# Optimization experiments

Hardware: AMD Instinct MI355X
Metric: run time of the kernel (lower is better)

The kernel has to match this reference:

```python
import jax, jax.numpy as jnp
import numpy as np
from math import factorial


def _su2_cg(j1, j2, j3, m1, m2, m3):
    # Complex SU(2) Clebsch-Gordan coefficient <j1 m1; j2 m2 | j3 m3> (Condon-Shortley),
    # same formula as e3nn's _su2_clebsch_gordan_coeff.
    if m3 != m1 + m2:
        return 0.0
    f = factorial
    vmin = max(-j1 + j2 + m3, -j1 + m1, 0)
    vmax = min(j2 + j3 + m1, j3 - j1 + j2, j3 + m3)
    C = ((2 * j3 + 1) * f(j3 + j1 - j2) * f(j3 - j1 + j2) * f(j1 + j2 - j3) / f(j1 + j2 + j3 + 1)
         * f(j3 + m3) * f(j3 - m3) / (f(j1 - m1) * f(j1 + m1) * f(j2 - m2) * f(j2 + m2))) ** 0.5
    S = 0.0
    for v in range(vmin, vmax + 1):
        S += (-1.0) ** (v + j2 + m2) / f(v) * f(j2 + j3 + m1 - v) * f(j1 - m1 + v) / (
            f(j3 - j1 + j2 - v) * f(j3 + m3 - v) * f(v + j1 - j2 - m3))
    return C * S


def _q(l):
    # Change of basis real -> complex spherical harmonics (e3nn convention).
    q = np.zeros((2 * l + 1, 2 * l + 1), dtype=np.complex128)
    for m in range(-l, 0):
        q[l + m, l + abs(m)] = 1 / 2 ** 0.5
        q[l + m, l - abs(m)] = -1j / 2 ** 0.5
    q[l, l] = 1
    for m in range(1, l + 1):
        q[l + m, l + abs(m)] = (-1) ** m / 2 ** 0.5
        q[l + m, l - abs(m)] = 1j * (-1) ** m / 2 ** 0.5
    return (-1j) ** l * q


def _w3j(l1, l2, l3):
    # Real Wigner-3j-like invariant tensor, Frobenius norm 1 (e3nn wigner_3j).
    C = np.zeros((2 * l1 + 1, 2 * l2 + 1, 2 * l3 + 1), dtype=np.complex128)
    for m1 in range(-l1, l1 + 1):
        for m2 in range(-l2, l2 + 1):
            m3 = m1 + m2
            if -l3 <= m3 <= l3:
                C[l1 + m1, l2 + m2, l3 + m3] = _su2_cg(l1, l2, l3, m1, m2, m3)
    C = np.einsum('ij,kl,mn,ikn->jlm', _q(l1), _q(l2), np.conj(_q(l3).T), C)
    C = np.real(C)
    return C / np.linalg.norm(C)


def _cg_full():
    # 1o x 1o -> 0e + 1e + 2e. e3nn FullTensorProduct ('uuu', component norm,
    # element path norm, mul=1) gives path_weight = sqrt(2*l_out + 1) per path.
    return np.concatenate([(2 * l + 1) ** 0.5 * _w3j(1, 1, l) for l in range(3)],
                          axis=-1).astype(np.float32)  # [3, 3, 9]


def setup_inputs() -> dict:
    key = jax.random.key(0)
    N = 8388608  # 2**23 rows, ~96 MB input
    frac = jax.random.normal(key, (N, 3), dtype=jnp.float32)
    cg = jnp.asarray(_cg_full())  # [3, 3, 9] fixed Clebsch-Gordan constants
    return {"frac": frac, "cg": cg}


def reference(frac, cg):
    # SimpleTP.forward: tp(frac, frac) -> [N, 9], then sum over dim 0 -> [9].
    # Fused segment-wise CG contraction + batch reduction in one einsum.
    return jnp.einsum('ni,nj,ijk->k', frac, frac, cg)
```

## Files before the change

kernel.cpp:

```cpp
#include <hip/hip_runtime.h>


constexpr int BLK  = 256;
constexpr int GRID = 2048;
constexpr int WPB  = BLK / 64;
constexpr long NWAVES = (long)GRID * WPB;

#define ACC6(x, y, z)                                              \
    do {                                                           \
        s00 = fmaf((x), (x), s00); s01 = fmaf((x), (y), s01);      \
        s02 = fmaf((x), (z), s02); s11 = fmaf((y), (y), s11);      \
        s12 = fmaf((y), (z), s12); s22 = fmaf((z), (z), s22);      \
    } while (0)

__global__ __launch_bounds__(BLK) void tp_partial(const float* __restrict__ frac,
                                                  float* __restrict__ ws,
                                                  long nchunks) {
    const int  lane = threadIdx.x & 63;
    const int  w    = threadIdx.x >> 6;
    const long wglb = (long)blockIdx.x * WPB + w;
    const float4* __restrict__ f4 = reinterpret_cast<const float4*>(frac);

    float s00 = 0.f, s01 = 0.f, s02 = 0.f, s11 = 0.f, s12 = 0.f, s22 = 0.f;

    for (long c = wglb; c < nchunks; c += NWAVES) {
        const long base = c * 768 + lane * 3;
        float4 v[12];
        #pragma unroll
        for (int s = 0; s < 4; ++s)
            #pragma unroll
            for (int k = 0; k < 3; ++k)
                v[s * 3 + k] = f4[base + 192 * s + k];

        #pragma unroll
        for (int s = 0; s < 4; ++s) {
            const float4 a = v[s * 3 + 0];
            const float4 b = v[s * 3 + 1];
            const float4 d = v[s * 3 + 2];
            ACC6(a.x, a.y, a.z);
            ACC6(a.w, b.x, b.y);
            ACC6(b.z, b.w, d.x);
            ACC6(d.y, d.z, d.w);
        }
    }

    #pragma unroll
    for (int off = 32; off > 0; off >>= 1) {
        s00 += __shfl_down(s00, off);
        s01 += __shfl_down(s01, off);
        s02 += __shfl_down(s02, off);
        s11 += __shfl_down(s11, off);
        s12 += __shfl_down(s12, off);
        s22 += __shfl_down(s22, off);
    }

    __shared__ float red[WPB][6];
    if (lane == 0) {
        red[w][0] = s00; red[w][1] = s01; red[w][2] = s02;
        red[w][3] = s11; red[w][4] = s12; red[w][5] = s22;
    }
    __syncthreads();
    if (threadIdx.x < 6) {
        float v = red[0][threadIdx.x] + red[1][threadIdx.x]
                + red[2][threadIdx.x] + red[3][threadIdx.x];
        ws[threadIdx.x * GRID + blockIdx.x] = v;
    }
}

__global__ __launch_bounds__(BLK) void tp_final(const float* __restrict__ frac,
                                                const float* __restrict__ ws,
                                                const float* __restrict__ cg,
                                                float* __restrict__ out,
                                                long tail_row, long nrows) {
    const float4* __restrict__ w4 = reinterpret_cast<const float4*>(ws);
    constexpr int Q = GRID / 4;

    float s[6];
    #pragma unroll
    for (int c = 0; c < 6; ++c) {
        float4 a = w4[c * Q + threadIdx.x];
        float4 b = w4[c * Q + threadIdx.x + BLK];
        s[c] = ((a.x + a.y) + (a.z + a.w)) + ((b.x + b.y) + (b.z + b.w));
    }

    for (long r = tail_row + threadIdx.x; r < nrows; r += BLK) {
        float x = frac[3 * r + 0], y = frac[3 * r + 1], z = frac[3 * r + 2];
        s[0] = fmaf(x, x, s[0]); s[1] = fmaf(x, y, s[1]); s[2] = fmaf(x, z, s[2]);
        s[3] = fmaf(y, y, s[3]); s[4] = fmaf(y, z, s[4]); s[5] = fmaf(z, z, s[5]);
    }

    #pragma unroll
    for (int off = 32; off > 0; off >>= 1) {
        #pragma unroll
        for (int c = 0; c < 6; ++c) s[c] += __shfl_down(s[c], off);
    }

    __shared__ float red[BLK / 64][6];
    const int lane = threadIdx.x & 63;
    const int wave = threadIdx.x >> 6;
    if (lane == 0) {
        #pragma unroll
        for (int c = 0; c < 6; ++c) red[wave][c] = s[c];
    }
    __syncthreads();

    __shared__ float M[9];
    if (threadIdx.x == 0) {
        float t[6];
        #pragma unroll
        for (int c = 0; c < 6; ++c)
            t[c] = red[0][c] + red[1][c] + red[2][c] + red[3][c];
        M[0] = t[0];  M[1] = t[1];  M[2] = t[2];
        M[3] = t[1];  M[4] = t[3];  M[5] = t[4];
        M[6] = t[2];  M[7] = t[4];  M[8] = t[5];
    }
    __syncthreads();

    if (threadIdx.x < 9) {
        const int k = threadIdx.x;
        float acc = 0.f;
        #pragma unroll
        for (int p = 0; p < 9; ++p)
            acc = fmaf(M[p], cg[p * 9 + k], acc);
        out[k] = acc;
    }
}

extern "C" void kernel_launch(void* const* d_in, const int* in_sizes, int n_in,
                              void* d_out, int out_size, void* d_ws, size_t ws_size,
                              hipStream_t stream) {
    const float* frac = (const float*)d_in[0];
    const float* cg   = (const float*)d_in[1];
    float*       out  = (float*)d_out;
    float*       ws   = (float*)d_ws;

    const long nfloats  = in_sizes[0];
    const long nrows    = nfloats / 3;
    const long nchunks  = nfloats / 3072;
    const long tail_row = nchunks * 1024;

    tp_partial<<<GRID, BLK, 0, stream>>>(frac, ws, nchunks);
    tp_final<<<1, BLK, 0, stream>>>(frac, ws, cg, out, tail_row, nrows);
}
```

Before: 22.98 us.

## Use fully coalesced float4 loads with cross-lane shuffles for row-boundary products

Each lane now loads consecutive float4s (stride 64 per q) instead of three adjacent float4s per lane, so every wave load instruction is fully contiguous. Since rows no longer align to lane boundaries, the kernel accumulates diagonal and off-diagonal products by phase (lane mod 3) and fetches the next lane's x/y via shuffles to complete rows that straddle float4s. This aims to improve memory coalescing on a bandwidth-bound reduction, at the cost of 24 shuffles per region and more complex index bookkeeping that must be exactly right.

New measurement: 23.54 us. +2.4%, slower.

```diff
diff --git a/kernel.cpp b/kernel.cpp
--- a/kernel.cpp
+++ b/kernel.cpp
@@ -6,43 +6,62 @@
 constexpr int WPB  = BLK / 64;
 constexpr long NWAVES = (long)GRID * WPB;
 
-#define ACC6(x, y, z)                                              \
-    do {                                                           \
-        s00 = fmaf((x), (x), s00); s01 = fmaf((x), (y), s01);      \
-        s02 = fmaf((x), (z), s02); s11 = fmaf((y), (y), s11);      \
-        s12 = fmaf((y), (z), s12); s22 = fmaf((z), (z), s22);      \
-    } while (0)
-
 __global__ __launch_bounds__(BLK) void tp_partial(const float* __restrict__ frac,
                                                   float* __restrict__ ws,
-                                                  long nchunks) {
+                                                  long nregions) {
     const int  lane = threadIdx.x & 63;
     const int  w    = threadIdx.x >> 6;
     const long wglb = (long)blockIdx.x * WPB + w;
     const float4* __restrict__ f4 = reinterpret_cast<const float4*>(frac);
 
-    float s00 = 0.f, s01 = 0.f, s02 = 0.f, s11 = 0.f, s12 = 0.f, s22 = 0.f;
+    const int  src  = (lane + 1) & 63;
+    const bool is63 = (lane == 63);
 
-    for (long c = wglb; c < nchunks; c += NWAVES) {
-        const long base = c * 768 + lane * 3;
+    float r[3] = {0.f, 0.f, 0.f};
+    float p[3] = {0.f, 0.f, 0.f};
+    float k[3] = {0.f, 0.f, 0.f};
+
+    for (long reg = wglb; reg < nregions; reg += NWAVES) {
+        const long base = reg * 768 + lane;
         float4 v[12];
         #pragma unroll
-        for (int s = 0; s < 4; ++s)
-            #pragma unroll
-            for (int k = 0; k < 3; ++k)
-                v[s * 3 + k] = f4[base + 192 * s + k];
+        for (int q = 0; q < 12; ++q)
+            v[q] = f4[base + 64 * q];
+
+        float rx[12], ry[12];
+        #pragma unroll
+        for (int q = 0; q < 12; ++q) {
+            rx[q] = __shfl(v[q].x, src);
+            ry[q] = __shfl(v[q].y, src);
+        }
 
         #pragma unroll
-        for (int s = 0; s < 4; ++s) {
-            const float4 a = v[s * 3 + 0];
-            const float4 b = v[s * 3 + 1];
-            const float4 d = v[s * 3 + 2];
-            ACC6(a.x, a.y, a.z);
-            ACC6(a.w, b.x, b.y);
-            ACC6(b.z, b.w, d.x);
-            ACC6(d.y, d.z, d.w);
+        for (int q = 0; q < 12; ++q) {
+            const float ex = (q < 11) ? (is63 ? rx[q + 1] : rx[q]) : rx[q];
+            const float ey = (q < 11) ? (is63 ? ry[q + 1] : ry[q]) : ry[q];
+            constexpr int D0[12] = {0,1,2,0,1,2,0,1,2,0,1,2};
+            const int d0 = D0[q], d1 = D0[(q + 1) % 12], d2 = D0[(q + 2) % 12];
+            const float h0 = v[q].x, h1 = v[q].y, h2 = v[q].z, h3 = v[q].w;
+            r[d0] = fmaf(h0, h0, r[d0]);
+            r[d1] = fmaf(h1, h1, r[d1]);
+            r[d2] = fmaf(h2, h2, r[d2]);
+            r[d0] = fmaf(h3, h3, r[d0]);
+            p[d0] = fmaf(h0, h1, p[d0]);
+            p[d1] = fmaf(h1, h2, p[d1]);
+            p[d2] = fmaf(h2, h3, p[d2]);
+            p[d0] = fmaf(h3, ex, p[d0]);
+            k[d0] = fmaf(h0, h2, k[d0]);
+            k[d1] = fmaf(h1, h3, k[d1]);
+            k[d2] = fmaf(h2, ex, k[d2]);
+            k[d0] = fmaf(h3, ey, k[d0]);
         }
     }
+
+    float s00, s01, s02, s11, s12, s22;
+    const int pl = lane % 3;
+    if (pl == 0)      { s00=r[0]; s11=r[1]; s22=r[2]; s01=p[0]; s12=p[1]; s02=k[0]; }
+    else if (pl == 1) { s00=r[2]; s11=r[0]; s22=r[1]; s01=p[2]; s12=p[0]; s02=k[2]; }
+    else              { s00=r[1]; s11=r[2]; s22=r[0]; s01=p[1]; s12=p[2]; s02=k[1]; }
 
     #pragma unroll
     for (int off = 32; off > 0; off >>= 1) {
@@ -117,12 +136,12 @@
     __syncthreads();
 
     if (threadIdx.x < 9) {
-        const int k = threadIdx.x;
+        const int kk = threadIdx.x;
         float acc = 0.f;
         #pragma unroll
-        for (int p = 0; p < 9; ++p)
-            acc = fmaf(M[p], cg[p * 9 + k], acc);
-        out[k] = acc;
+        for (int pth = 0; pth < 9; ++pth)
+            acc = fmaf(M[pth], cg[pth * 9 + kk], acc);
+        out[kk] = acc;
     }
 }
 
@@ -134,11 +153,11 @@
     float*       out  = (float*)d_out;
     float*       ws   = (float*)d_ws;
 
-    const long nfloats  = in_sizes[0];
-    const long nrows    = nfloats / 3;
-    const long nchunks  = nfloats / 3072;
-    const long tail_row = nchunks * 1024;
+    const long nfloats   = in_sizes[0];
+    const long nrows     = nfloats / 3;
+    const long nregions  = nfloats / 3072;
+    const long tail_row  = nregions * 1024;
 
-    tp_partial<<<GRID, BLK, 0, stream>>>(frac, ws, nchunks);
+    tp_partial<<<GRID, BLK, 0, stream>>>(frac, ws, nregions);
     tp_final<<<1, BLK, 0, stream>>>(frac, ws, cg, out, tail_row, nrows);
 }
```
